# Performance work log

Hardware: AMD Instinct MI355X
Metric: run time of the kernel (lower is better)

Reference implementation:

```python
import jax, jax.numpy as jnp
import numpy as np

# Material constants (from init_kwargs: E=1e4, nu=0.3)
E_MOD = 1.0e4
NU = 0.3
MU = E_MOD / (2.0 * (1.0 + NU))                      # shear modulus
LMBDA = E_MOD * NU / ((1.0 + NU) * (1.0 - 2.0 * NU))  # first Lame parameter
EPS = 1e-10

B, N_NODES, N_ELEM, N_QUAD, NPE = 4, 100000, 500000, 4, 4  # tet4 mesh


def setup_inputs() -> dict:
    key = jax.random.key(0)
    k1, k2, k3, k4 = jax.random.split(key, 4)
    # small displacements so J = det(I + grad_u) stays positive
    u = jax.random.normal(k1, (B, N_NODES, 3), dtype=jnp.float32) * 0.01
    elements = jax.random.randint(k2, (N_ELEM, NPE), 0, N_NODES)
    # precomputed shape-function derivatives dN/dx per element/quad point
    dN_dx = jax.random.normal(k3, (N_ELEM, N_QUAD, NPE, 3), dtype=jnp.float32) * 0.1
    # positive Jacobian determinants of the reference->physical map
    detJ = jax.random.uniform(k4, (N_ELEM, N_QUAD), dtype=jnp.float32, minval=0.5, maxval=1.5) * 1e-3
    # tet4 4-point quadrature weights: 0.25 / 6
    quad_weights = jnp.full((N_QUAD,), 0.25 / 6.0, dtype=jnp.float32)
    return {"u": u, "elements": elements, "dN_dx": dN_dx, "detJ": detJ,
            "quad_weights": quad_weights}


def reference(u, elements, dN_dx, detJ, quad_weights):
    # gather nodal displacements per element: [B, E, n, 3]
    elem_u = u[:, elements]
    # grad_u[b,e,q,i,j] = sum_n elem_u[b,e,n,i] * dN_dx[e,q,n,j]  -> [B,E,Q,3,3]
    grad_u = jnp.einsum('beni,eqnj->beqij', elem_u, dN_dx)
    F = grad_u + jnp.eye(3, dtype=u.dtype)
    J = jnp.linalg.det(F)                      # [B,E,Q]
    I_C = jnp.sum(F * F, axis=(-2, -1))        # tr(F^T F)
    logJ = jnp.log(jnp.maximum(J, EPS))
    W = 0.5 * MU * (I_C - 3.0 - 2.0 * logJ) + 0.25 * LMBDA * (J * J - 1.0 - 2.0 * logJ)
    # quadrature-weighted assembly over elements and quad points -> [B]
    return jnp.einsum('beq,eq,q->b', W, detJ, quad_weights)
```

## Files before the change

### kernel.cpp

```cpp
#include <hip/hip_runtime.h>

#define MU_C   3846.1538461538462f
#define LM_C   5769.2307692307695f
#define LOGC   (MU_C + 0.5f * LM_C)
#define EPS_C  1e-10f

#define PBLOCKS 2048

__global__ __launch_bounds__(256) void nh_transpose_u_pad(
    const float* __restrict__ u, float4* __restrict__ ut, int n_nodes)
{
    const int i = blockIdx.x * 256 + threadIdx.x;
    if (i >= n_nodes) return;
    float4* q = ut + (size_t)i * 4;
    #pragma unroll
    for (int b = 0; b < 4; ++b) {
        const float* p = u + ((size_t)b * n_nodes + i) * 3;
        q[b] = make_float4(p[0], p[1], p[2], 0.f);
    }
}

__device__ __forceinline__ float nh_energy(
    const float4* dn,
    const float4* uu,
    const float*  wqv)
{
    const float* d  = reinterpret_cast<const float*>(dn);
    const float* us = reinterpret_cast<const float*>(uu);
    float a = 0.f;
    #pragma unroll
    for (int q = 0; q < 4; ++q) {
        float F[3][3];
        #pragma unroll
        for (int i = 0; i < 3; ++i) {
            #pragma unroll
            for (int j = 0; j < 3; ++j) {
                float g = 0.f;
                #pragma unroll
                for (int n = 0; n < 4; ++n)
                    g = fmaf(us[n * 4 + i], d[(q*4 + n)*3 + j], g);
                F[i][j] = g + ((i == j) ? 1.f : 0.f);
            }
        }
        const float J =
              F[0][0] * (F[1][1]*F[2][2] - F[1][2]*F[2][1])
            - F[0][1] * (F[1][0]*F[2][2] - F[1][2]*F[2][0])
            + F[0][2] * (F[1][0]*F[2][1] - F[1][1]*F[2][0]);
        float IC = 0.f;
        #pragma unroll
        for (int i = 0; i < 3; ++i)
            #pragma unroll
            for (int j = 0; j < 3; ++j)
                IC = fmaf(F[i][j], F[i][j], IC);
        const float lj = __logf(fmaxf(J, EPS_C));
        const float W = 0.5f * MU_C * (IC - 3.f)
                      + 0.25f * LM_C * fmaf(J, J, -1.f)
                      - LOGC * lj;
        a = fmaf(W, wqv[q], a);
    }
    return a;
}

__global__ __launch_bounds__(256) void nh_partial_v8(
    const float4* __restrict__ ut,
    const int*    __restrict__ elements,
    const float*  __restrict__ dN_dx,
    const float*  __restrict__ detJ,
    const float*  __restrict__ qw,
    float* __restrict__ partial,
    int n_elem, int ntiles)
{
    const int t = threadIdx.x;
    const int b = t & 3;
    const int p = t >> 2;

    const int4*   elp = reinterpret_cast<const int4*>(elements);
    const float4* djp = reinterpret_cast<const float4*>(detJ);
    const float4* dnp = reinterpret_cast<const float4*>(dN_dx);
    const float4  w4  = *reinterpret_cast<const float4*>(qw);

    float acc = 0.f;

    for (int tile = blockIdx.x; tile < ntiles; tile += gridDim.x) {
        const int e = tile * 64 + p;
        if (e >= n_elem) continue;

        const int4   nd = elp[e];
        const float4 dj = djp[e];

        float4 dv[12];
        const float4* dptr = dnp + (size_t)e * 12;
        #pragma unroll
        for (int k = 0; k < 12; ++k) dv[k] = dptr[k];

        float4 uu[4];
        uu[0] = ut[nd.x * 4 + b];
        uu[1] = ut[nd.y * 4 + b];
        uu[2] = ut[nd.z * 4 + b];
        uu[3] = ut[nd.w * 4 + b];

        const float wqv[4] = {dj.x * w4.x, dj.y * w4.y, dj.z * w4.z, dj.w * w4.w};

        acc += nh_energy(dv, uu, wqv);
    }

    #pragma unroll
    for (int off = 32; off >= 4; off >>= 1)
        acc += __shfl_down(acc, off);

    __shared__ float s_red[4][4];
    const int lane = t & 63;
    const int wid  = t >> 6;
    if (lane < 4) s_red[wid][lane] = acc;
    __syncthreads();
    if (t < 4)
        partial[(size_t)blockIdx.x * 4 + t] =
            (s_red[0][t] + s_red[1][t]) + (s_red[2][t] + s_red[3][t]);
}

__global__ __launch_bounds__(256) void nh_final(
    const float* __restrict__ partial,
    float* __restrict__ out,
    int nparts)
{
    float accb[4] = {0.f, 0.f, 0.f, 0.f};
    for (int i = threadIdx.x; i < nparts; i += 256) {
        const float4 p = reinterpret_cast<const float4*>(partial)[i];
        accb[0] += p.x; accb[1] += p.y; accb[2] += p.z; accb[3] += p.w;
    }

    #pragma unroll
    for (int b = 0; b < 4; ++b) {
        float v = accb[b];
        #pragma unroll
        for (int off = 32; off > 0; off >>= 1)
            v += __shfl_down(v, off);
        accb[b] = v;
    }

    __shared__ float lds[4][4];
    const int lane = threadIdx.x & 63;
    const int wid  = threadIdx.x >> 6;
    if (lane == 0) {
        #pragma unroll
        for (int b = 0; b < 4; ++b) lds[wid][b] = accb[b];
    }
    __syncthreads();
    if (threadIdx.x == 0) {
        #pragma unroll
        for (int b = 0; b < 4; ++b)
            out[b] = (lds[0][b] + lds[1][b]) + (lds[2][b] + lds[3][b]);
    }
}

extern "C" void kernel_launch(void* const* d_in, const int* in_sizes, int n_in,
                              void* d_out, int out_size, void* d_ws, size_t ws_size,
                              hipStream_t stream) {
    const float* u        = (const float*)d_in[0];
    const int*   elements = (const int*)d_in[1];
    const float* dN_dx    = (const float*)d_in[2];
    const float* detJ     = (const float*)d_in[3];
    const float* qw       = (const float*)d_in[4];
    float* out = (float*)d_out;

    const int B       = out_size;
    const int n_nodes = in_sizes[0] / (3 * B);
    const int n_elem  = in_sizes[1] / 4;

    const int threads = 256;
    const int ntiles  = (n_elem + 63) / 64;
    const int nblocks = (ntiles < PBLOCKS) ? ntiles : PBLOCKS;

    const size_t ut_bytes = (size_t)n_nodes * 4 * sizeof(float4);
    float4* ut     = (float4*)d_ws;
    float* partial = (float*)((char*)d_ws + ut_bytes);

    const int tb = (n_nodes + threads - 1) / threads;
    nh_transpose_u_pad<<<tb, threads, 0, stream>>>(u, ut, n_nodes);

    nh_partial_v8<<<nblocks, threads, 0, stream>>>(ut, elements, dN_dx, detJ, qw,
                                                   partial, n_elem, ntiles);
    nh_final<<<1, threads, 0, stream>>>(partial, out, nblocks);
}
```

Baseline: 61.47 us.

## Stage dN_dx tiles through padded LDS with double-buffered software pipeline

The main kernel now assigns each block a contiguous chunk of tiles. It loads each tile's dN_dx with coalesced float4 reads into a padded, double-buffered shared-memory slab, with element indices and detJ staged alongside. It prefetches the next tile's data and gathers the next element's displacement vectors while computing the current tile. Grid size drops to 1024 blocks and an occupancy hint is added. The aim is to hide global-memory latency and replace strided per-thread 192-byte loads with coalesced ones. The cost is extra LDS traffic, a barrier every tile and higher register pressure.

```diff
diff --git a/kernel.cpp b/kernel.cpp
--- a/kernel.cpp
+++ b/kernel.cpp
@@ -5,7 +5,7 @@
 #define LOGC   (MU_C + 0.5f * LM_C)
 #define EPS_C  1e-10f
 
-#define PBLOCKS 2048
+#define NB_TARGET 1024
 
 __global__ __launch_bounds__(256) void nh_transpose_u_pad(
     const float* __restrict__ u, float4* __restrict__ ut, int n_nodes)
@@ -20,16 +20,21 @@
     }
 }
 
-__device__ __forceinline__ float nh_energy(
-    const float4* dn,
-    const float4* uu,
-    const float*  wqv)
-{
-    const float* d  = reinterpret_cast<const float*>(dn);
-    const float* us = reinterpret_cast<const float*>(uu);
+__device__ __forceinline__ float nh_energy_lds(
+    const float4* slab,
+    const float4& u0, const float4& u1, const float4& u2, const float4& u3,
+    const float* wq)
+{
+    const float un[4][3] = {{u0.x, u0.y, u0.z}, {u1.x, u1.y, u1.z},
+                            {u2.x, u2.y, u2.z}, {u3.x, u3.y, u3.z}};
     float a = 0.f;
     #pragma unroll
     for (int q = 0; q < 4; ++q) {
+        const float4 f0 = slab[q*3 + 0];
+        const float4 f1 = slab[q*3 + 1];
+        const float4 f2 = slab[q*3 + 2];
+        const float d[12] = {f0.x,f0.y,f0.z,f0.w, f1.x,f1.y,f1.z,f1.w,
+                             f2.x,f2.y,f2.z,f2.w};
         float F[3][3];
         #pragma unroll
         for (int i = 0; i < 3; ++i) {
@@ -38,7 +43,7 @@
                 float g = 0.f;
                 #pragma unroll
                 for (int n = 0; n < 4; ++n)
-                    g = fmaf(us[n * 4 + i], d[(q*4 + n)*3 + j], g);
+                    g = fmaf(un[n][i], d[n*3 + j], g);
                 F[i][j] = g + ((i == j) ? 1.f : 0.f);
             }
         }
@@ -56,59 +61,125 @@
         const float W = 0.5f * MU_C * (IC - 3.f)
                       + 0.25f * LM_C * fmaf(J, J, -1.f)
                       - LOGC * lj;
-        a = fmaf(W, wqv[q], a);
+        a = fmaf(W, wq[q], a);
     }
     return a;
 }
 
-__global__ __launch_bounds__(256) void nh_partial_v8(
+__global__ __launch_bounds__(256, 4) void nh_partial_v9(
     const float4* __restrict__ ut,
-    const int*    __restrict__ elements,
-    const float*  __restrict__ dN_dx,
-    const float*  __restrict__ detJ,
+    const int4*   __restrict__ elp,
+    const float4* __restrict__ dnp,
+    const float4* __restrict__ djp,
     const float*  __restrict__ qw,
     float* __restrict__ partial,
-    int n_elem, int ntiles)
-{
+    int n_elem, int ntiles, int chunk)
+{
+    __shared__ float4 s_dn[2][64 * 13];
+    __shared__ float4 s_dj[2][64];
+    __shared__ int4   s_el[3][64];
+    __shared__ float  s_red[4][4];
+
     const int t = threadIdx.x;
     const int b = t & 3;
     const int p = t >> 2;
 
-    const int4*   elp = reinterpret_cast<const int4*>(elements);
-    const float4* djp = reinterpret_cast<const float4*>(detJ);
-    const float4* dnp = reinterpret_cast<const float4*>(dN_dx);
-    const float4  w4  = *reinterpret_cast<const float4*>(qw);
+    const int t0  = blockIdx.x * chunk;
+    const int t1  = min(t0 + chunk, ntiles);
+    const int cnt = t1 - t0;
+
+    if (cnt <= 0) {
+        if (t < 4) partial[(size_t)blockIdx.x * 4 + t] = 0.f;
+        return;
+    }
+
+    const int tlast  = t1 - 1;
+    const int nf4max = n_elem * 12 - 1;
+    const int nelmax = n_elem - 1;
+    const float4 w4  = *reinterpret_cast<const float4*>(qw);
+
+    const int oA = (t       / 12) * 13 + (t       % 12);
+    const int oB = ((t+256) / 12) * 13 + ((t+256) % 12);
+    const int oC = ((t+512) / 12) * 13 + ((t+512) % 12);
 
     float acc = 0.f;
 
-    for (int tile = blockIdx.x; tile < ntiles; tile += gridDim.x) {
-        const int e = tile * 64 + p;
-        if (e >= n_elem) continue;
-
-        const int4   nd = elp[e];
-        const float4 dj = djp[e];
-
-        float4 dv[12];
-        const float4* dptr = dnp + (size_t)e * 12;
-        #pragma unroll
-        for (int k = 0; k < 12; ++k) dv[k] = dptr[k];
-
-        float4 uu[4];
-        uu[0] = ut[nd.x * 4 + b];
-        uu[1] = ut[nd.y * 4 + b];
-        uu[2] = ut[nd.z * 4 + b];
-        uu[3] = ut[nd.w * 4 + b];
-
-        const float wqv[4] = {dj.x * w4.x, dj.y * w4.y, dj.z * w4.z, dj.w * w4.w};
-
-        acc += nh_energy(dv, uu, wqv);
-    }
+    {
+        float4 r0, r1, r2, rdj; int4 rel0, rel1;
+        const int base = t0 * 768;
+        r0 = dnp[min(base + t,       nf4max)];
+        r1 = dnp[min(base + t + 256, nf4max)];
+        r2 = dnp[min(base + t + 512, nf4max)];
+        if (t < 64) {
+            rel0 = elp[min(t0 * 64 + t, nelmax)];
+            rel1 = elp[min(min(t0 + 1, tlast) * 64 + t, nelmax)];
+        } else if (t < 128) {
+            rdj = djp[min(t0 * 64 + (t - 64), nelmax)];
+        }
+        s_dn[0][oA] = r0; s_dn[0][oB] = r1; s_dn[0][oC] = r2;
+        if (t < 64)       { s_el[0][t] = rel0; s_el[1][t] = rel1; }
+        else if (t < 128) { s_dj[0][t - 64] = rdj; }
+        __syncthreads();
+    }
+
+    float4 uA0, uA1, uA2, uA3, uB0, uB1, uB2, uB3;
+    {
+        const int4 nd = s_el[0][p];
+        uA0 = ut[nd.x * 4 + b]; uA1 = ut[nd.y * 4 + b];
+        uA2 = ut[nd.z * 4 + b]; uA3 = ut[nd.w * 4 + b];
+    }
+
+    #define NH_BODY(M, CC, U0,U1,U2,U3, V0,V1,V2,V3)                          \
+    {                                                                         \
+               \
+        const int tn  = min(t0 + (M) + 1, tlast);                             \
+        const int te2 = min(t0 + (M) + 2, tlast);                             \
+        float4 r0, r1, r2, rdj; int4 rel;                                     \
+        {                                                                     \
+            const int base = tn * 768;                                        \
+            r0 = dnp[min(base + t,       nf4max)];                            \
+            r1 = dnp[min(base + t + 256, nf4max)];                            \
+            r2 = dnp[min(base + t + 512, nf4max)];                            \
+            if (t < 64)       rel = elp[min(te2 * 64 + t, nelmax)];           \
+            else if (t < 128) rdj = djp[min(tn * 64 + (t - 64), nelmax)];     \
+        }                                                                     \
+        __builtin_amdgcn_sched_barrier(0);                                    \
+                             \
+        {                                                                     \
+            const int4 nd = s_el[((M) + 1) % 3][p];                           \
+            V0 = ut[nd.x * 4 + b]; V1 = ut[nd.y * 4 + b];                     \
+            V2 = ut[nd.z * 4 + b]; V3 = ut[nd.w * 4 + b];                     \
+        }                                                                     \
+        __builtin_amdgcn_sched_barrier(0);                                    \
+                                           \
+        {                                                                     \
+            const int tile = t0 + (M);                                        \
+            const float sc = ((M) < cnt && tile * 64 + p < n_elem) ? 1.f : 0.f;\
+            const float4 dj4 = s_dj[CC][p];                                   \
+            const float wq[4] = {dj4.x * w4.x * sc, dj4.y * w4.y * sc,        \
+                                 dj4.z * w4.z * sc, dj4.w * w4.w * sc};       \
+            acc += nh_energy_lds(&s_dn[CC][p * 13], U0, U1, U2, U3, wq);      \
+        }                                                                     \
+                           \
+        s_dn[(CC) ^ 1][oA] = r0;                                              \
+        s_dn[(CC) ^ 1][oB] = r1;                                              \
+        s_dn[(CC) ^ 1][oC] = r2;                                              \
+        if (t < 64)       s_el[((M) + 2) % 3][t] = rel;                       \
+        else if (t < 128) s_dj[(CC) ^ 1][t - 64] = rdj;                       \
+        __syncthreads();                                                      \
+    }
+
+    const int iters = (cnt + 1) & ~1;
+    for (int m = 0; m < iters; m += 2) {
+        NH_BODY(m,     0, uA0,uA1,uA2,uA3, uB0,uB1,uB2,uB3)
+        NH_BODY(m + 1, 1, uB0,uB1,uB2,uB3, uA0,uA1,uA2,uA3)
+    }
+    #undef NH_BODY
 
     #pragma unroll
     for (int off = 32; off >= 4; off >>= 1)
         acc += __shfl_down(acc, off);
 
-    __shared__ float s_red[4][4];
     const int lane = t & 63;
     const int wid  = t >> 6;
     if (lane < 4) s_red[wid][lane] = acc;
@@ -169,7 +240,8 @@
 
     const int threads = 256;
     const int ntiles  = (n_elem + 63) / 64;
-    const int nblocks = (ntiles < PBLOCKS) ? ntiles : PBLOCKS;
+    const int nblocks = (ntiles < NB_TARGET) ? ntiles : NB_TARGET;
+    const int chunk   = (ntiles + nblocks - 1) / nblocks;
 
     const size_t ut_bytes = (size_t)n_nodes * 4 * sizeof(float4);
     float4* ut     = (float4*)d_ws;
@@ -178,7 +250,11 @@
     const int tb = (n_nodes + threads - 1) / threads;
     nh_transpose_u_pad<<<tb, threads, 0, stream>>>(u, ut, n_nodes);
 
-    nh_partial_v8<<<nblocks, threads, 0, stream>>>(ut, elements, dN_dx, detJ, qw,
-                                                   partial, n_elem, ntiles);
+    nh_partial_v9<<<nblocks, threads, 0, stream>>>(
+        ut, reinterpret_cast<const int4*>(elements),
+        reinterpret_cast<const float4*>(dN_dx),
+        reinterpret_cast<const float4*>(detJ),
+        qw, partial, n_elem, ntiles, chunk);
+
     nh_final<<<1, threads, 0, stream>>>(partial, out, nblocks);
 }
```

After: 133.1 us. +116.5%, slower.

## Software-pipeline element loads with double buffering over contiguous tile chunks

Applied to the files above, without the earlier changes.

Each block now handles a contiguous run of tiles instead of a grid-stride loop. The loads for the next tile (connectivity, dN_dx, detJ and gathered displacements) go into a second register buffer and are issued while the current tile's energy is computed, hiding gather latency. The grid is halved to 1024 blocks and out-of-range elements are clamped and masked by a zero weight. The cost is much higher register pressure from two 12-float4 buffers, which may lower occupancy.

```diff
diff --git a/kernel.cpp b/kernel.cpp
--- a/kernel.cpp
+++ b/kernel.cpp
@@ -5,7 +5,7 @@
 #define LOGC   (MU_C + 0.5f * LM_C)
 #define EPS_C  1e-10f
 
-#define PBLOCKS 2048
+#define NBLK 1024
 
 __global__ __launch_bounds__(256) void nh_transpose_u_pad(
     const float* __restrict__ u, float4* __restrict__ ut, int n_nodes)
@@ -61,54 +61,67 @@
     return a;
 }
 
-__global__ __launch_bounds__(256) void nh_partial_v8(
+__global__ __launch_bounds__(256) void nh_partial_v10(
     const float4* __restrict__ ut,
-    const int*    __restrict__ elements,
-    const float*  __restrict__ dN_dx,
-    const float*  __restrict__ detJ,
+    const int4*   __restrict__ elp,
+    const float4* __restrict__ dnp,
+    const float4* __restrict__ djp,
     const float*  __restrict__ qw,
     float* __restrict__ partial,
-    int n_elem, int ntiles)
+    int n_elem, int ntiles, int chunk)
 {
     const int t = threadIdx.x;
     const int b = t & 3;
     const int p = t >> 2;
-
-    const int4*   elp = reinterpret_cast<const int4*>(elements);
-    const float4* djp = reinterpret_cast<const float4*>(detJ);
-    const float4* dnp = reinterpret_cast<const float4*>(dN_dx);
-    const float4  w4  = *reinterpret_cast<const float4*>(qw);
+    const int t0  = blockIdx.x * chunk;
+    const int cnt = min(chunk, ntiles - t0);
+
+    __shared__ float s_red[4][4];
 
     float acc = 0.f;
 
-    for (int tile = blockIdx.x; tile < ntiles; tile += gridDim.x) {
-        const int e = tile * 64 + p;
-        if (e >= n_elem) continue;
-
-        const int4   nd = elp[e];
-        const float4 dj = djp[e];
-
-        float4 dv[12];
-        const float4* dptr = dnp + (size_t)e * 12;
-        #pragma unroll
-        for (int k = 0; k < 12; ++k) dv[k] = dptr[k];
-
-        float4 uu[4];
-        uu[0] = ut[nd.x * 4 + b];
-        uu[1] = ut[nd.y * 4 + b];
-        uu[2] = ut[nd.z * 4 + b];
-        uu[3] = ut[nd.w * 4 + b];
-
-        const float wqv[4] = {dj.x * w4.x, dj.y * w4.y, dj.z * w4.z, dj.w * w4.w};
-
-        acc += nh_energy(dv, uu, wqv);
+    if (cnt > 0) {
+        const float4 w4 = *reinterpret_cast<const float4*>(qw);
+        const int nelmax = n_elem - 1;
+
+        float4 dnA[12], dnB[12];
+        float4 uuA[4],  uuB[4];
+        float  wqA[4],  wqB[4];
+
+        #define NH_LOAD(DN, UU, WQ, M)                                        \
+        {                                                                     \
+            const int e  = (t0 + (M)) * 64 + p;                               \
+            const int ec = min(e, nelmax);                                    \
+            const int4   nd = elp[ec];                                        \
+            const float4 dj = djp[ec];                                        \
+            const float4* dptr = dnp + (size_t)ec * 12;                       \
+            _Pragma("unroll")                                                 \
+            for (int k = 0; k < 12; ++k) DN[k] = dptr[k];                     \
+            UU[0] = ut[nd.x * 4 + b];                                         \
+            UU[1] = ut[nd.y * 4 + b];                                         \
+            UU[2] = ut[nd.z * 4 + b];                                         \
+            UU[3] = ut[nd.w * 4 + b];                                         \
+            const float vs = (e < n_elem) ? 1.f : 0.f;                        \
+            WQ[0] = dj.x * w4.x * vs; WQ[1] = dj.y * w4.y * vs;               \
+            WQ[2] = dj.z * w4.z * vs; WQ[3] = dj.w * w4.w * vs;               \
+        }
+
+        NH_LOAD(dnA, uuA, wqA, 0)
+        if (cnt > 1) NH_LOAD(dnB, uuB, wqB, 1)
+
+        for (int m = 0; m < cnt; m += 2) {
+            acc += nh_energy(dnA, uuA, wqA);
+            if (m + 2 < cnt) NH_LOAD(dnA, uuA, wqA, m + 2)
+            if (m + 1 < cnt) acc += nh_energy(dnB, uuB, wqB);
+            if (m + 3 < cnt) NH_LOAD(dnB, uuB, wqB, m + 3)
+        }
+        #undef NH_LOAD
     }
 
     #pragma unroll
     for (int off = 32; off >= 4; off >>= 1)
         acc += __shfl_down(acc, off);
 
-    __shared__ float s_red[4][4];
     const int lane = t & 63;
     const int wid  = t >> 6;
     if (lane < 4) s_red[wid][lane] = acc;
@@ -169,7 +182,8 @@
 
     const int threads = 256;
     const int ntiles  = (n_elem + 63) / 64;
-    const int nblocks = (ntiles < PBLOCKS) ? ntiles : PBLOCKS;
+    const int nblocks = (ntiles < NBLK) ? ntiles : NBLK;
+    const int chunk   = (ntiles + nblocks - 1) / nblocks;
 
     const size_t ut_bytes = (size_t)n_nodes * 4 * sizeof(float4);
     float4* ut     = (float4*)d_ws;
@@ -178,7 +192,11 @@
     const int tb = (n_nodes + threads - 1) / threads;
     nh_transpose_u_pad<<<tb, threads, 0, stream>>>(u, ut, n_nodes);
 
-    nh_partial_v8<<<nblocks, threads, 0, stream>>>(ut, elements, dN_dx, detJ, qw,
-                                                   partial, n_elem, ntiles);
+    nh_partial_v10<<<nblocks, threads, 0, stream>>>(
+        ut, reinterpret_cast<const int4*>(elements),
+        reinterpret_cast<const float4*>(dN_dx),
+        reinterpret_cast<const float4*>(detJ),
+        qw, partial, n_elem, ntiles, chunk);
+
     nh_final<<<1, threads, 0, stream>>>(partial, out, nblocks);
 }
```

Result: faster. 58.24 us (-5.3%).
